# Performance work log

Hardware: AMD Instinct MI355X
Metric: run time of the kernel (lower is better)

Reference implementation:

```python
import jax, jax.numpy as jnp
import numpy as np
import math

B, S, D = 2, 2048, 3072
H, KVH = 24, 8
HD = D // H  # 128
N_REP = H // KVH  # 3


def setup_inputs() -> dict:
    key = jax.random.key(0)
    ks = jax.random.split(key, 8)
    x = jax.random.normal(ks[0], (B, S, D), dtype=jnp.float32)
    # RoPE frequencies: cos/sin of theta-scaled angles (real/imag of freqs_cis)
    theta = 500000.0
    inv_freq = 1.0 / (theta ** (np.arange(0, HD, 2, dtype=np.float32) / HD))  # (HD/2,)
    t = np.arange(S, dtype=np.float32)
    ang = np.outer(t, inv_freq)  # (S, HD/2)
    freqs_cos = jnp.asarray(np.cos(ang), dtype=jnp.float32)
    freqs_sin = jnp.asarray(np.sin(ang), dtype=jnp.float32)
    # additive causal mask (1,1,S,S)
    mask = jnp.where(jnp.tril(jnp.ones((S, S), dtype=bool)), 0.0, -1e9).astype(jnp.float32)[None, None]
    scale = 0.02
    wq = jax.random.normal(ks[1], (H * HD, D), dtype=jnp.float32) * scale
    wk = jax.random.normal(ks[2], (KVH * HD, D), dtype=jnp.float32) * scale
    wv = jax.random.normal(ks[3], (KVH * HD, D), dtype=jnp.float32) * scale
    wo = jax.random.normal(ks[4], (D, H * HD), dtype=jnp.float32) * scale
    return {"x": x, "freqs_cos": freqs_cos, "freqs_sin": freqs_sin, "mask": mask,
            "wq": wq, "wk": wk, "wv": wv, "wo": wo}


def _rotate_half(t):
    h = t.shape[-1] // 2
    return jnp.concatenate([-t[..., h:], t[..., :h]], axis=-1)


def reference(x, freqs_cos, freqs_sin, mask, wq, wk, wv, wo):
    b, s, _ = x.shape
    xq = (x @ wq.T).reshape(b, s, H, HD)
    xk = (x @ wk.T).reshape(b, s, KVH, HD)
    xv = (x @ wv.T).reshape(b, s, KVH, HD)
    # RoPE: cos/sin duplicated along last dim, broadcast over batch & heads
    cos = jnp.concatenate([freqs_cos, freqs_cos], axis=-1)[None, :, None, :]  # (1,S,1,HD)
    sin = jnp.concatenate([freqs_sin, freqs_sin], axis=-1)[None, :, None, :]
    xq = xq * cos + _rotate_half(xq) * sin
    xk = xk * cos + _rotate_half(xk) * sin
    # GQA: repeat_interleave KV heads (k0,k0,k0,k1,...) matches jnp.repeat
    keys = jnp.repeat(xk, N_REP, axis=2)    # (B,S,H,HD)
    values = jnp.repeat(xv, N_REP, axis=2)
    scores = jnp.einsum('bqhd,bkhd->bhqk', xq, keys) / math.sqrt(HD)
    scores = scores + mask
    attn = jax.nn.softmax(scores.astype(jnp.float32), axis=-1).astype(xq.dtype)
    out = jnp.einsum('bhqk,bkhd->bqhd', attn, values).reshape(b, s, H * HD)
    return out @ wo.T
```

## Files before the change

kernel.cpp:

```cpp
#include <hip/hip_runtime.h>

typedef unsigned short u16;
typedef unsigned int u32;
typedef __attribute__((ext_vector_type(8))) __bf16 bf16x8;
typedef __attribute__((ext_vector_type(4))) float f32x4;
typedef __attribute__((ext_vector_type(4))) u32 u32x4;
typedef __attribute__((ext_vector_type(8))) u16 u16x8;
typedef __attribute__((ext_vector_type(4))) u16 u16x4;

#define S_LEN 2048
#define DM 3072
#define NH 24
#define NKV 8

__device__ __forceinline__ u16 f2b(float f) {
  u32 u = __builtin_bit_cast(u32, f);
  u = u + 0x7FFFu + ((u >> 16) & 1u);
  return (u16)(u >> 16);
}
__device__ __forceinline__ float b2f(u16 h) {
  u32 u = ((u32)h) << 16;
  return __builtin_bit_cast(float, u);
}
__device__ __forceinline__ f32x4 mfma16(bf16x8 a, bf16x8 b, f32x4 c) {
  return __builtin_amdgcn_mfma_f32_16x16x32_bf16(a, b, c, 0, 0, 0);
}
__device__ __forceinline__ void gload16(const u16* g, u16* l) {
  __builtin_amdgcn_global_load_lds((const __attribute__((address_space(1))) void*)g,
                                   (__attribute__((address_space(3))) void*)l, 16, 0, 0);
}

__device__ __forceinline__ void cvt_one(const float* __restrict__ s, u16* __restrict__ d, int j) {
  const f32x4* p = (const f32x4*)(s + (size_t)j * 8);
  f32x4 a = p[0], b = p[1];
  u16x8 o;
#pragma unroll
  for (int q = 0; q < 4; ++q) { o[q] = f2b(a[q]); o[q + 4] = f2b(b[q]); }
  *(u16x8*)(d + (size_t)j * 8) = o;
}
__global__ __launch_bounds__(256) void cvt4_kernel(const float* __restrict__ s0, u16* __restrict__ d0,
                                                   const float* __restrict__ s1, u16* __restrict__ d1,
                                                   const float* __restrict__ s2, u16* __restrict__ d2,
                                                   const float* __restrict__ s3, u16* __restrict__ d3) {
  int i = blockIdx.x * 256 + threadIdx.x;
  if (i < 1572864)      cvt_one(s0, d0, i);
  else if (i < 2752512) cvt_one(s1, d1, i - 1572864);
  else if (i < 3145728) cvt_one(s2, d2, i - 2752512);
  else                  cvt_one(s3, d3, i - 3145728);
}

__device__ __forceinline__ void swz_bid(int& bx, int& by) {
  int gx = gridDim.x;
  int tot = gx * gridDim.y;
  int id = blockIdx.y * gx + blockIdx.x;
  int cpx = tot >> 3;
  int s = (id & 7) * cpx + (id >> 3);
  bx = s % gx;
  by = s / gx;
}

template <int BN>
__device__ __forceinline__ void gemm256_body(u16* __restrict__ lds,
                                             const u16* __restrict__ A, const u16* __restrict__ B,
                                             void* __restrict__ Cv, int N, int K,
                                             int m0, int n0, int mode) {
  constexpr int NJ = BN / 64;
  constexpr int NSB = BN / 64;
  constexpr int BBUF = NSB * 4096;
  const int tid = threadIdx.x;
  const int lane = tid & 63;
  const int w = tid >> 6;
  const int l15 = lane & 15, g = lane >> 4;
  const int wm = w >> 2, wn = w & 3;
  const int srow = tid >> 3;
  const int scol = ((tid & 7) ^ (srow & 7)) * 8;
  const u16* aS = A + (size_t)(m0 + srow) * K + scol;
  const u16* bS = B + (size_t)(n0 + srow) * K + scol;
  const int sdst = (tid & 448) * 8;
  const int swz0 = (g ^ (l15 & 7)) * 8;
  const int swz1 = ((4 + g) ^ (l15 & 7)) * 8;
  const int aB0 = wm * 8192 + l15 * 64;
  const int bB0 = wn * (BN / 4) * 64 + l15 * 64;

  f32x4 acc[8][NJ];
#pragma unroll
  for (int i = 0; i < 8; ++i)
#pragma unroll
    for (int j = 0; j < NJ; ++j) acc[i][j] = 0.f;

  auto stage = [&](int k0, int bsel) {
#pragma unroll
    for (int s = 0; s < 4; ++s)
      gload16(aS + (size_t)(s * 64) * K + k0, lds + bsel * 16384 + s * 4096 + sdst);
#pragma unroll
    for (int s = 0; s < NSB; ++s)
      gload16(bS + (size_t)(s * 64) * K + k0, lds + 32768 + bsel * BBUF + s * 4096 + sdst);
  };

  stage(0, 0);
  asm volatile("s_waitcnt vmcnt(0)" ::: "memory");
  __builtin_amdgcn_s_barrier();

  for (int t = 0; t < 48; ++t) {
    const int bsel = t & 1;
    const u16* ldsA = lds + bsel * 16384 + aB0;
    const u16* ldsB = lds + 32768 + bsel * BBUF + bB0;
    bf16x8 af[4], bf[NJ];
#pragma unroll
    for (int i = 0; i < 4; ++i) af[i] = *(const bf16x8*)(ldsA + i * 1024 + swz0);
#pragma unroll
    for (int j = 0; j < NJ; ++j) bf[j] = *(const bf16x8*)(ldsB + j * 1024 + swz0);
    if (t < 47) stage((t + 1) * 64, bsel ^ 1);
    asm volatile("" ::: "memory");
    __builtin_amdgcn_s_barrier();
    asm volatile("s_waitcnt lgkmcnt(0)" ::: "memory");
    __builtin_amdgcn_sched_barrier(0);
    __builtin_amdgcn_s_setprio(1);
#pragma unroll
    for (int i = 0; i < 4; ++i)
#pragma unroll
      for (int j = 0; j < NJ; ++j) acc[i][j] = mfma16(af[i], bf[j], acc[i][j]);
    __builtin_amdgcn_s_setprio(0);
    asm volatile("" ::: "memory");
    __builtin_amdgcn_s_barrier();
#pragma unroll
    for (int i = 0; i < 4; ++i) af[i] = *(const bf16x8*)(ldsA + (4 + i) * 1024 + swz0);
    asm volatile("" ::: "memory");
    __builtin_amdgcn_s_barrier();
    asm volatile("s_waitcnt lgkmcnt(0)" ::: "memory");
    __builtin_amdgcn_sched_barrier(0);
    __builtin_amdgcn_s_setprio(1);
#pragma unroll
    for (int i = 0; i < 4; ++i)
#pragma unroll
      for (int j = 0; j < NJ; ++j) acc[4 + i][j] = mfma16(af[i], bf[j], acc[4 + i][j]);
    __builtin_amdgcn_s_setprio(0);
    asm volatile("" ::: "memory");
    __builtin_amdgcn_s_barrier();
#pragma unroll
    for (int i = 0; i < 4; ++i) af[i] = *(const bf16x8*)(ldsA + i * 1024 + swz1);
#pragma unroll
    for (int j = 0; j < NJ; ++j) bf[j] = *(const bf16x8*)(ldsB + j * 1024 + swz1);
    asm volatile("" ::: "memory");
    __builtin_amdgcn_s_barrier();
    asm volatile("s_waitcnt lgkmcnt(0)" ::: "memory");
    __builtin_amdgcn_sched_barrier(0);
    __builtin_amdgcn_s_setprio(1);
#pragma unroll
    for (int i = 0; i < 4; ++i)
#pragma unroll
      for (int j = 0; j < NJ; ++j) acc[i][j] = mfma16(af[i], bf[j], acc[i][j]);
    __builtin_amdgcn_s_setprio(0);
    asm volatile("" ::: "memory");
    __builtin_amdgcn_s_barrier();
#pragma unroll
    for (int i = 0; i < 4; ++i) af[i] = *(const bf16x8*)(ldsA + (4 + i) * 1024 + swz1);
    asm volatile("" ::: "memory");
    asm volatile("s_waitcnt vmcnt(0)" ::: "memory");
    __builtin_amdgcn_s_barrier();
    asm volatile("s_waitcnt lgkmcnt(0)" ::: "memory");
    __builtin_amdgcn_sched_barrier(0);
    __builtin_amdgcn_s_setprio(1);
#pragma unroll
    for (int i = 0; i < 4; ++i)
#pragma unroll
      for (int j = 0; j < NJ; ++j) acc[4 + i][j] = mfma16(af[i], bf[j], acc[4 + i][j]);
    __builtin_amdgcn_s_setprio(0);
    asm volatile("" ::: "memory");
    __builtin_amdgcn_s_barrier();
  }
#pragma unroll
  for (int i = 0; i < 8; ++i)
#pragma unroll
    for (int j = 0; j < NJ; ++j) {
      int nn = n0 + wn * (BN / 4) + j * 16 + l15;
      int mmb = m0 + wm * 128 + i * 16 + g * 4;
      if (mode == 1) {
#pragma unroll
        for (int r = 0; r < 4; ++r)
          ((float*)Cv)[(size_t)(mmb + r) * N + nn] = acc[i][j][r];
      } else if (mode == 0) {
#pragma unroll
        for (int r = 0; r < 4; ++r)
          ((u16*)Cv)[(size_t)(mmb + r) * N + nn] = f2b(acc[i][j][r]);
      } else {
        u16x4 pk;
#pragma unroll
        for (int r = 0; r < 4; ++r) pk[r] = f2b(acc[i][j][r]);
        *(u16x4*)((u16*)Cv + (size_t)nn * 2048 + (size_t)(mmb >> 11) * 2097152 + (mmb & 2047)) = pk;
      }
    }
}

__global__ __launch_bounds__(512, 1) void gemm_qkv(const u16* __restrict__ A,
                                                   const u16* __restrict__ Bq, u16* __restrict__ Cq,
                                                   const u16* __restrict__ Bk, const u16* __restrict__ Bv,
                                                   u16* __restrict__ Ck, u16* __restrict__ Cv, int K) {
  __shared__ __align__(16) u16 lds[57344];
  int id = blockIdx.x;
  if (id < 256) {
    int s = (id & 7) * 32 + (id >> 3);
    gemm256_body<192>(lds, A, Bq, Cq, 3072, K, (s / 16) * 256, (s % 16) * 192, 0);
  } else {
    id -= 256;
    int s = (id & 7) * 32 + (id >> 3);
    int bx = s % 16, by = s / 16;
    bool isv = bx >= 8;
    gemm256_body<128>(lds, A, isv ? Bv : Bk, isv ? Cv : Ck, 1024, K, by * 256, (bx & 7) * 128,
                      isv ? 2 : 0);
  }
}
__global__ __launch_bounds__(512, 1) void gemm192_f32(const u16* __restrict__ A, const u16* __restrict__ B,
                                                      float* __restrict__ C, int N, int K) {
  __shared__ __align__(16) u16 lds[57344];
  int bx, by; swz_bid(bx, by);
  gemm256_body<192>(lds, A, B, C, N, K, by * 256, bx * 192, 1);
}

__global__ __launch_bounds__(256) void rope_kernel(u16* __restrict__ t, const float* __restrict__ fc,
                                                   const float* __restrict__ fs, int nheads, int total) {
  int idx = blockIdx.x * 256 + threadIdx.x;
  if (idx >= total) return;
  int c = idx & 7;
  int tmp = idx >> 3;
  int h = tmp % nheads;
  int row = tmp / nheads;
  int s = row & (S_LEN - 1);
  int d0 = c << 3;
  u16* base = t + (size_t)row * (nheads * 128) + h * 128;
  u16x8 lo = *(const u16x8*)(base + d0);
  u16x8 hi = *(const u16x8*)(base + 64 + d0);
  const float* cp = fc + s * 64 + d0;
  const float* sp = fs + s * 64 + d0;
  u16x8 olo, ohi;
#pragma unroll
  for (int j = 0; j < 8; ++j) {
    float cv = cp[j], sn = sp[j];
    float a = b2f(lo[j]), b = b2f(hi[j]);
    olo[j] = f2b(a * cv - b * sn);
    ohi[j] = f2b(b * cv + a * sn);
  }
  *(u16x8*)(base + d0) = olo;
  *(u16x8*)(base + 64 + d0) = ohi;
}

__global__ __launch_bounds__(256, 2) void attn_kernel(const u16* __restrict__ xq,
                                                      const u16* __restrict__ xk,
                                                      const u16* __restrict__ xvT,
                                                      const float* __restrict__ fc,
                                                      const float* __restrict__ fs,
                                                      u16* __restrict__ o,
                                                      const float* __restrict__ wo,
                                                      u16* __restrict__ wob) {
  __shared__ __align__(16) u16 smem[40960];
  if (blockIdx.x >= 768) {
    int i = (blockIdx.x - 768) * 256 + threadIdx.x;
    cvt_one(wo, wob, i);
    return;
  }
  const int tid = threadIdx.x;
  const int w = tid >> 6, lane = tid & 63;
  const int l15 = lane & 15, g = lane >> 4;
  const int id = blockIdx.x;
  const int xcd = id & 7, slot = id >> 3;
  const int grp = xcd + 8 * (slot / 48);
  const int s48 = slot % 48;
  const int b = grp >> 3, kvh = grp & 7;
  const int qb = 15 - s48 / 3;
  const int h = kvh * 3 + s48 % 3;
  const float sc2 = 0.08838834764831845f * 1.4426950408889634f;

  const u16* ksrc = xk + (size_t)b * 2097152 + kvh * 128;
  const u16* vsrc = xvT + (size_t)(b * 1024 + kvh * 128) * 2048;
  int koff[4], vofs[4], dst4[4];
#pragma unroll
  for (int r = 0; r < 4; ++r) {
    int c = r * 256 + tid;
    int krow = c >> 4, kj = (c & 15) ^ (krow & 7);
    koff[r] = krow * 1024 + kj * 8;
    int vrow = c >> 3, vj = (c & 7) ^ (vrow & 7);
    vofs[r] = vrow * 2048 + vj * 8;
    dst4[r] = (r * 256 + (tid & 192)) * 8;
  }
  u16* sPw = smem + 32768 + w * 2048;
  const int pxr = (l15 & 7) << 3;

  const int q0 = qb * 128;

  bf16x8 qf[2][4];
#pragma unroll
  for (int s = 0; s < 2; ++s) {
    const int qrow = q0 + w * 32 + s * 16 + l15;
    const u16* qptr = xq + (size_t)(b * S_LEN + qrow) * DM + h * 128;
#pragma unroll
    for (int dcp = 0; dcp < 2; ++dcp) {
      u16x8 Lo = *(const u16x8*)(qptr + dcp * 32 + g * 8);
      u16x8 Hi = *(const u16x8*)(qptr + 64 + dcp * 32 + g * 8);
      const float* cp = fc + qrow * 64 + dcp * 32 + g * 8;
      const float* sp = fs + qrow * 64 + dcp * 32 + g * 8;
      bf16x8 qlo, qhi;
#pragma unroll
      for (int j = 0; j < 8; ++j) {
        float cv = cp[j], sn = sp[j];
        float a = b2f(Lo[j]), bb = b2f(Hi[j]);
        qlo[j] = (__bf16)((a * cv - bb * sn) * sc2);
        qhi[j] = (__bf16)((bb * cv + a * sn) * sc2);
      }
      qf[s][dcp] = qlo;
      qf[s][dcp + 2] = qhi;
    }
  }

  u16 *sKc = smem, *sKn = smem + 8192;
  u16 *sVc = smem + 16384, *sVn = smem + 24576;

  f32x4 accO[2][8];
#pragma unroll
  for (int s = 0; s < 2; ++s)
#pragma unroll
    for (int i = 0; i < 8; ++i) accO[s][i] = 0.f;
  float m_[2] = {-1e30f, -1e30f}, ls_[2] = {0.f, 0.f};
  const int nt = 2 * qb + 2;

#pragma unroll
  for (int r = 0; r < 4; ++r) gload16(ksrc + koff[r], sKc + dst4[r]);
#pragma unroll
  for (int r = 0; r < 4; ++r) gload16(vsrc + vofs[r], sVc + dst4[r]);
  __syncthreads();

  for (int t = 0; t < nt; ++t) {
    if (t + 1 < nt) {
      int k0n = (t + 1) * 64;
#pragma unroll
      for (int r = 0; r < 4; ++r) gload16(ksrc + (size_t)k0n * 1024 + koff[r], sKn + dst4[r]);
#pragma unroll
      for (int r = 0; r < 4; ++r) gload16(vsrc + k0n + vofs[r], sVn + dst4[r]);
    }
    if (64 * t <= q0 + w * 32 + 31) {
      f32x4 st[2][4];
      __builtin_amdgcn_s_setprio(1);
#pragma unroll
      for (int kt = 0; kt < 4; ++kt) {
        int row = kt * 16 + l15;
        bf16x8 kf[4];
#pragma unroll
        for (int dc = 0; dc < 4; ++dc)
          kf[dc] = *(const bf16x8*)(sKc + row * 128 + ((dc * 32 + g * 8) ^ ((row & 7) << 3)));
        f32x4 a0 = 0.f, a1 = 0.f;
#pragma unroll
        for (int dc = 0; dc < 4; ++dc) {
          a0 = mfma16(kf[dc], qf[0][dc], a0);
          a1 = mfma16(kf[dc], qf[1][dc], a1);
        }
        st[0][kt] = a0;
        st[1][kt] = a1;
      }
      __builtin_amdgcn_s_setprio(0);
#pragma unroll
      for (int s = 0; s < 2; ++s) {
        const int qrow = q0 + w * 32 + s * 16 + l15;
        float pmax = -1e30f;
#pragma unroll
        for (int kt = 0; kt < 4; ++kt)
#pragma unroll
          for (int r = 0; r < 4; ++r) {
            float x = st[s][kt][r];
            if (t >= nt - 2) {
              int kk = t * 64 + kt * 16 + g * 4 + r;
              if (kk > qrow) x = -1e30f;
            }
            st[s][kt][r] = x;
            pmax = fmaxf(pmax, x);
          }
        pmax = fmaxf(pmax, __shfl_xor(pmax, 16));
        pmax = fmaxf(pmax, __shfl_xor(pmax, 32));
        if (!__all(pmax - m_[s] <= 8.0f)) {
          float mnew = fmaxf(m_[s], pmax);
          float corr = exp2f(m_[s] - mnew);
          ls_[s] *= corr;
#pragma unroll
          for (int i = 0; i < 8; ++i) accO[s][i] *= corr;
          m_[s] = mnew;
        }
        float ps = 0.f;
#pragma unroll
        for (int kt = 0; kt < 4; ++kt) {
          u16x4 pk;
#pragma unroll
          for (int r = 0; r < 4; ++r) {
            float p = exp2f(st[s][kt][r] - m_[s]);
            ps += p;
            pk[r] = f2b(p);
          }
          *(u16x4*)(sPw + s * 1024 + ((l15 * 64 + kt * 16 + g * 4) ^ pxr)) = pk;
        }
        ps += __shfl_xor(ps, 16);
        ps += __shfl_xor(ps, 32);
        ls_[s] += ps;
      }
      bf16x8 pf[2][2];
#pragma unroll
      for (int s = 0; s < 2; ++s)
#pragma unroll
        for (int ck = 0; ck < 2; ++ck)
          pf[s][ck] = *(const bf16x8*)(sPw + s * 1024 + ((l15 * 64 + ck * 32 + g * 8) ^ pxr));
      __builtin_amdgcn_s_setprio(1);
#pragma unroll
      for (int dt = 0; dt < 8; ++dt) {
        int row = dt * 16 + l15;
#pragma unroll
        for (int ck = 0; ck < 2; ++ck) {
          bf16x8 vf = *(const bf16x8*)(sVc + row * 64 + ((ck * 32 + g * 8) ^ ((row & 7) << 3)));
          accO[0][dt] = mfma16(vf, pf[0][ck], accO[0][dt]);
          accO[1][dt] = mfma16(vf, pf[1][ck], accO[1][dt]);
        }
      }
      __builtin_amdgcn_s_setprio(0);
    }
    __syncthreads();
    u16* tk = sKc; sKc = sKn; sKn = tk;
    u16* tv = sVc; sVc = sVn; sVn = tv;
  }
  u16* sOw = smem + w * 8192;
#pragma unroll
  for (int s = 0; s < 2; ++s) {
    float invl = 1.0f / ls_[s];
#pragma unroll
    for (int dt = 0; dt < 8; ++dt)
#pragma unroll
      for (int r = 0; r < 4; ++r) {
        int d = dt * 16 + g * 4 + r;
        sOw[((s * 16 + l15) * 128 + d) ^ pxr] = f2b(accO[s][dt][r] * invl);
      }
  }
#pragma unroll
  for (int p = 0; p < 8; ++p) {
    int idx = p * 64 + lane;
    int q = idx >> 4, c = idx & 15;
    int j = c ^ (q & 7);
    u32x4 v = *(const u32x4*)(sOw + q * 128 + j * 8);
    *(u32x4*)(o + (size_t)(b * S_LEN + q0 + w * 32 + q) * DM + h * 128 + c * 8) = v;
  }
}

extern "C" void kernel_launch(void* const* d_in, const int* in_sizes, int n_in,
                              void* d_out, int out_size, void* d_ws, size_t ws_size,
                              hipStream_t stream) {
  const float* x  = (const float*)d_in[0];
  const float* fc = (const float*)d_in[1];
  const float* fs = (const float*)d_in[2];
  const float* wq = (const float*)d_in[4];
  const float* wk = (const float*)d_in[5];
  const float* wv = (const float*)d_in[6];
  const float* wo = (const float*)d_in[7];
  float* out = (float*)d_out;
  char* ws = (char*)d_ws;

  u16* xb  = (u16*)(ws);
  u16* wqb = (u16*)(ws + 25165824);
  u16* att = (u16*)(ws + 25165824);
  u16* wkb = (u16*)(ws + 44040192);
  u16* wvb = (u16*)(ws + 50331648);
  u16* xqb = (u16*)(ws + 56623104);
  u16* xkb = (u16*)(ws + 81788928);
  u16* xvT = (u16*)(ws + 90177536);
  u16* wob = (u16*)(ws);

  cvt4_kernel<<<13824, 256, 0, stream>>>(x, xb, wq, wqb, wk, wkb, wv, wvb);

  gemm_qkv<<<512, 512, 0, stream>>>(xb, wqb, xqb, wkb, wvb, xkb, xvT, 3072);

  rope_kernel<<<1024, 256, 0, stream>>>(xkb, fc, fs, NKV, 4096 * NKV * 8);

  attn_kernel<<<5376, 256, 0, stream>>>(xqb, xkb, xvT, fc, fs, att, wo, wob);

  gemm192_f32<<<dim3(16, 16), 512, 0, stream>>>(att, wob, out, 3072, 3072);
}
```

Measured before the change: 341.4 us.

## Fuse Q/K/V projections into one 320-wide tiled GEMM over concatenated weights

Replaces the two-variant QKV GEMM launch (512 blocks mixing 192-wide Q tiles and 128-wide K/V tiles) with 256 uniform blocks of 256x320 tiles over the contiguous wq/wk/wv bf16 buffer. The epilogue routes each column to Q, K or transposed V by its index. The goal is one full wave of equal-sized blocks across the CUs, better A-tile reuse per block and no second partial wave. In exchange each block uses more LDS and more accumulator registers, and the epilogue gains per-column branching.

```diff
diff --git a/kernel.cpp b/kernel.cpp
--- a/kernel.cpp
+++ b/kernel.cpp
@@ -63,7 +63,9 @@
 __device__ __forceinline__ void gemm256_body(u16* __restrict__ lds,
                                              const u16* __restrict__ A, const u16* __restrict__ B,
                                              void* __restrict__ Cv, int N, int K,
-                                             int m0, int n0, int mode) {
+                                             int m0, int n0, int mode,
+                                             void* __restrict__ C2 = nullptr,
+                                             void* __restrict__ C3 = nullptr) {
   constexpr int NJ = BN / 64;
   constexpr int NSB = BN / 64;
   constexpr int BBUF = NSB * 4096;
@@ -183,32 +185,41 @@
 #pragma unroll
         for (int r = 0; r < 4; ++r)
           ((u16*)Cv)[(size_t)(mmb + r) * N + nn] = f2b(acc[i][j][r]);
-      } else {
+      } else if (mode == 2) {
         u16x4 pk;
 #pragma unroll
         for (int r = 0; r < 4; ++r) pk[r] = f2b(acc[i][j][r]);
         *(u16x4*)((u16*)Cv + (size_t)nn * 2048 + (size_t)(mmb >> 11) * 2097152 + (mmb & 2047)) = pk;
+      } else {
+        if (nn < 3072) {
+#pragma unroll
+          for (int r = 0; r < 4; ++r)
+            ((u16*)Cv)[(size_t)(mmb + r) * 3072 + nn] = f2b(acc[i][j][r]);
+        } else if (nn < 4096) {
+#pragma unroll
+          for (int r = 0; r < 4; ++r)
+            ((u16*)C2)[(size_t)(mmb + r) * 1024 + (nn - 3072)] = f2b(acc[i][j][r]);
+        } else {
+          int d = nn - 4096;
+          u16x4 pk;
+#pragma unroll
+          for (int r = 0; r < 4; ++r) pk[r] = f2b(acc[i][j][r]);
+          *(u16x4*)((u16*)C3 + (size_t)d * 2048 + (size_t)(mmb >> 11) * 2097152 + (mmb & 2047)) = pk;
+        }
       }
     }
 }
 
 __global__ __launch_bounds__(512, 1) void gemm_qkv(const u16* __restrict__ A,
-                                                   const u16* __restrict__ Bq, u16* __restrict__ Cq,
-                                                   const u16* __restrict__ Bk, const u16* __restrict__ Bv,
-                                                   u16* __restrict__ Ck, u16* __restrict__ Cv, int K) {
-  __shared__ __align__(16) u16 lds[57344];
+                                                   const u16* __restrict__ Wcat,
+                                                   u16* __restrict__ Cq,
+                                                   u16* __restrict__ Ck, u16* __restrict__ Cv,
+                                                   int K) {
+  __shared__ __align__(16) u16 lds[73728];
   int id = blockIdx.x;
-  if (id < 256) {
-    int s = (id & 7) * 32 + (id >> 3);
-    gemm256_body<192>(lds, A, Bq, Cq, 3072, K, (s / 16) * 256, (s % 16) * 192, 0);
-  } else {
-    id -= 256;
-    int s = (id & 7) * 32 + (id >> 3);
-    int bx = s % 16, by = s / 16;
-    bool isv = bx >= 8;
-    gemm256_body<128>(lds, A, isv ? Bv : Bk, isv ? Cv : Ck, 1024, K, by * 256, (bx & 7) * 128,
-                      isv ? 2 : 0);
-  }
+  int s = (id & 7) * 32 + (id >> 3);
+  int by = s >> 4, c = s & 15;
+  gemm256_body<320>(lds, A, Wcat, Cq, 0, K, by * 256, c * 320, 3, Ck, Cv);
 }
 __global__ __launch_bounds__(512, 1) void gemm192_f32(const u16* __restrict__ A, const u16* __restrict__ B,
                                                       float* __restrict__ C, int N, int K) {
@@ -468,7 +479,7 @@
 
   cvt4_kernel<<<13824, 256, 0, stream>>>(x, xb, wq, wqb, wk, wkb, wv, wvb);
 
-  gemm_qkv<<<512, 512, 0, stream>>>(xb, wqb, xqb, wkb, wvb, xkb, xvT, 3072);
+  gemm_qkv<<<256, 512, 0, stream>>>(xb, wqb, xqb, xkb, xvT, 3072);
 
   rope_kernel<<<1024, 256, 0, stream>>>(xkb, fc, fs, NKV, 4096 * NKV * 8);
 
```

After: 328.6 us. 1.04x faster.
